# Kernel tuning notes

Measured on AMD Instinct MI355X. Metric: run time of the kernel, lower is better.

The kernel has to match this reference:

```python
import jax, jax.numpy as jnp
import numpy as np

ALPHA_MGD = 2e-05
NOISE_SIGMA = 8.0
NOISE_VAR = NOISE_SIGMA ** 2  # 64.0


def _conv2d(x, w, b, pad):
    # x: [N,C,H,W], w: [O,I,kh,kw]
    y = jax.lax.conv_general_dilated(
        x, w, window_strides=(1, 1), padding=[(pad, pad), (pad, pad)],
        dimension_numbers=("NCHW", "OIHW", "NCHW"))
    return y + b[None, :, None, None]


def setup_inputs() -> dict:
    key = jax.random.key(0)
    ks = jax.random.split(key, 8)
    N, Cs, Ct, H, W = 8, 128, 256, 64, 64
    return {
        "preds_S": jax.random.normal(ks[0], (N, Cs, H, W), jnp.float32),
        "preds_T": jax.random.normal(ks[1], (N, Ct, H, W), jnp.float32),
        "W_align": jax.random.normal(ks[2], (Ct, Cs, 1, 1), jnp.float32) * 0.05,
        "b_align": jnp.zeros((Ct,), jnp.float32),
        "W_gen1": jax.random.normal(ks[3], (Ct, Ct, 3, 3), jnp.float32) * 0.02,
        "b_gen1": jnp.zeros((Ct,), jnp.float32),
        "W_gen2": jax.random.normal(ks[4], (Ct, Ct, 3, 3), jnp.float32) * 0.02,
        "b_gen2": jnp.zeros((Ct,), jnp.float32),
    }


def reference(preds_S, preds_T, W_align, b_align, W_gen1, b_gen1, W_gen2, b_gen2):
    # align student channels to teacher channels (1x1 conv)
    s = _conv2d(preds_S, W_align, b_align, pad=0)
    N, C, H, W = preds_T.shape
    # deterministic checkerboard mask: tile([[0,1],[1,0]]) cropped to HxW -> (h+w) % 2
    hh = jnp.arange(H)[:, None]
    ww = jnp.arange(W)[None, :]
    mat = ((hh + ww) % 2).astype(s.dtype)  # [H,W]
    masked_fea = s * mat  # broadcast over [N,C,H,W]
    # generation network: conv3x3 -> relu -> conv3x3
    new_fea = _conv2d(jax.nn.relu(_conv2d(masked_fea, W_gen1, b_gen1, pad=1)), W_gen2, b_gen2, pad=1)
    # bmc_loss_md(pred=preds_T, target=new_fea, noise_var=64):
    # logits[i,j] = MVN(pred_i, noise_var*I).log_prob(target_j); the normalization
    # constant is class-independent and cancels in cross-entropy, keep the quadratic term.
    p = preds_T.reshape(N, -1)   # [N, D], D = C*H*W
    t = new_fea.reshape(N, -1)   # [N, D]
    # pairwise squared L2 via ||p||^2 + ||t||^2 - 2 p.t  (avoids NxNxD blow-up)
    sq = (jnp.sum(p * p, axis=1)[:, None]
          + jnp.sum(t * t, axis=1)[None, :]
          - 2.0 * (p @ t.T))  # [N, N]
    logits = -0.5 * sq / NOISE_VAR
    # cross_entropy(logits, arange(N)) = mean_i (logsumexp_j logits[i,j] - logits[i,i])
    ce = jnp.mean(jax.nn.logsumexp(logits, axis=1) - jnp.diagonal(logits))
    loss = ce * (2.0 * NOISE_VAR) / N
    return loss * ALPHA_MGD
```

## Files before the change

kernel.cpp:

```cpp
#include <hip/hip_runtime.h>

typedef unsigned short u16;
typedef short short8 __attribute__((ext_vector_type(8)));
typedef unsigned short ushort8 __attribute__((ext_vector_type(8)));
typedef float floatx16 __attribute__((ext_vector_type(16)));

#define PLANE8   34848
#define NSTRIDE  1115136

__device__ __forceinline__ u16 f2b(float f) {
  unsigned u = __builtin_bit_cast(unsigned, f);
  return (u16)((u + 0x7FFFu + ((u >> 16) & 1u)) >> 16);
}
__device__ __forceinline__ float b2f(u16 b) {
  return __builtin_bit_cast(float, ((unsigned)b) << 16);
}

typedef const __attribute__((address_space(1))) unsigned int* gptr_t;
typedef __attribute__((address_space(3))) unsigned int* sptr_t;

__global__ __launch_bounds__(256) void kprep(
    const float* __restrict__ Wg1, u16* __restrict__ Wsw1,
    const float* __restrict__ Wg2, u16* __restrict__ Wsw2,
    const float* __restrict__ Wa,  u16* __restrict__ Wb,
    const float* __restrict__ pS,  u16* __restrict__ T,
    u16* __restrict__ masked, u16* __restrict__ t1)
{
  __shared__ u16 Ls[64 * 136];
  int b = blockIdx.x, t = threadIdx.x;

  if (b < 576) {
    const float* W = (b < 288) ? Wg1 : Wg2;
    u16* D = (b < 288) ? Wsw1 : Wsw2;
    int bb = (b < 288) ? b : b - 288;
    int cid = bb * 256 + t;
    int d = cid % 1152, ctcg = cid / 1152;
    int ct = ctcg & 3, cg = ctcg >> 2;
    int colow = d & 31, cihalf = (d >> 5) & 1, sc = (d >> 6) & 1, tap = d >> 7;
    int co = ct * 64 + sc * 32 + colow;
    short8 v;
    #pragma unroll
    for (int jj = 0; jj < 8; ++jj) {
      int ci = cg * 16 + cihalf * 8 + jj;
      v[jj] = (short)f2b(W[((size_t)(co * 256 + ci)) * 9 + tap]);
    }
    *(short8*)&D[(size_t)cid * 8] = v;
  } else if (b < 592) {
    int v = (b - 576) * 256 + t;
    int colow = v & 31, hfb = (v >> 5) & 1, cog = (v >> 6) & 7, k = v >> 9;
    int co = cog * 32 + colow;
    int ci0 = k * 16 + hfb * 8;
    float4 f0 = *(const float4*)(Wa + (size_t)co * 128 + ci0);
    float4 f1 = *(const float4*)(Wa + (size_t)co * 128 + ci0 + 4);
    short8 o;
    o[0] = (short)f2b(f0.x); o[1] = (short)f2b(f0.y);
    o[2] = (short)f2b(f0.z); o[3] = (short)f2b(f0.w);
    o[4] = (short)f2b(f1.x); o[5] = (short)f2b(f1.y);
    o[6] = (short)f2b(f1.z); o[7] = (short)f2b(f1.w);
    *(short8*)&Wb[(size_t)v * 8] = o;
  } else if (b < 1104) {
    int bb = b - 592;
    int n = bb >> 6, pt = bb & 63, pix0 = pt * 64;
    int ci = t >> 1, ph = t & 1;
    const float* src = pS + ((size_t)n * 128 + ci) * 4096 + pix0 + ph * 32;
    #pragma unroll
    for (int i = 0; i < 8; ++i) {
      float4 v4 = *(const float4*)(src + i * 4);
      int pix = ph * 32 + i * 4;
      Ls[(pix + 0) * 136 + ci] = f2b(v4.x);
      Ls[(pix + 1) * 136 + ci] = f2b(v4.y);
      Ls[(pix + 2) * 136 + ci] = f2b(v4.z);
      Ls[(pix + 3) * 136 + ci] = f2b(v4.w);
    }
    __syncthreads();
    int p = t >> 2, q = t & 3;
    const u16* row = Ls + p * 136 + q * 32;
    u16* dst = T + ((size_t)n * 4096 + pix0 + p) * 128 + q * 32;
    #pragma unroll
    for (int k2 = 0; k2 < 4; ++k2)
      *(ushort8*)(dst + k2 * 8) = *(const ushort8*)(row + k2 * 8);
  } else {
    int p = b - 1104;
    u16* base = ((p >> 8) ? t1 : masked);
    int q = p & 255;
    base += (size_t)(q >> 5) * NSTRIDE + (size_t)(q & 31) * PLANE8;
    short8 z;
    #pragma unroll
    for (int jj = 0; jj < 8; ++jj) z[jj] = 0;
    #pragma unroll
    for (int pass = 0; pass < 2; ++pass) {
      int seg = t + pass * 256;
      if (seg < 264) {
        int off;
        if (seg < 66)       off = seg * 8;
        else if (seg < 132) off = (65 * 66 + (seg - 66)) * 8;
        else if (seg < 198) off = ((seg - 132) * 66) * 8;
        else                off = ((seg - 198) * 66 + 65) * 8;
        *(short8*)(base + off) = z;
      }
    }
  }
}

__global__ __launch_bounds__(256) void k1m(const u16* __restrict__ T,
    const u16* __restrict__ Wb, const float* __restrict__ ba,
    u16* __restrict__ mk)
{
  __shared__ __align__(16) u16 Wl[32768];
  int b = blockIdx.x;
  int n = b >> 5, pt = b & 31;
  int t = threadIdx.x, wid = t >> 6, lane = t & 63;
  int ml = lane & 31, hf = lane >> 5;

  #pragma unroll
  for (int kk = 0; kk < 16; ++kk) {
    int chunk = kk * 256 + t;
    __builtin_amdgcn_global_load_lds((gptr_t)(const void*)(Wb + (size_t)chunk * 8),
                                     (sptr_t)(void*)(Wl + chunk * 8), 16, 0, 0);
  }

  const u16* Tn = T + (size_t)n * 524288;
  const u16* ap[4];
  #pragma unroll
  for (int g = 0; g < 4; ++g)
    ap[g] = Tn + (size_t)(pt * 128 + g * 32 + ml) * 128 + hf * 8;

  floatx16 acc[2][4];
  #pragma unroll
  for (int q = 0; q < 2; ++q)
    #pragma unroll
    for (int g = 0; g < 4; ++g)
      #pragma unroll
      for (int i = 0; i < 16; ++i) acc[q][g][i] = 0.f;

  __syncthreads();

  const short8* WlV = (const short8*)Wl;
  int cogb = wid * 2;

  short8 a0[4], a1[4];
  #pragma unroll
  for (int g = 0; g < 4; ++g) a0[g] = *(const short8*)(ap[g]);

#define K1M_STEP(K, CUR, NXT, LAST)                                           \
  {                                                                           \
    if (!(LAST)) {                                                            \
      _Pragma("unroll")                                                       \
      for (int g = 0; g < 4; ++g)                                             \
        NXT[g] = *(const short8*)(ap[g] + ((K) + 1) * 16);                    \
    }                                                                         \
    short8 w0 = WlV[((K) * 8 + cogb) * 64 + lane];                            \
    short8 w1 = WlV[((K) * 8 + cogb + 1) * 64 + lane];                        \
    _Pragma("unroll")                                                         \
    for (int g = 0; g < 4; ++g) {                                             \
      acc[0][g] = __builtin_amdgcn_mfma_f32_32x32x16_bf16(CUR[g], w0, acc[0][g], 0, 0, 0); \
      acc[1][g] = __builtin_amdgcn_mfma_f32_32x32x16_bf16(CUR[g], w1, acc[1][g], 0, 0, 0); \
    }                                                                         \
  }
  K1M_STEP(0, a0, a1, 0)
  K1M_STEP(1, a1, a0, 0)
  K1M_STEP(2, a0, a1, 0)
  K1M_STEP(3, a1, a0, 0)
  K1M_STEP(4, a0, a1, 0)
  K1M_STEP(5, a1, a0, 0)
  K1M_STEP(6, a0, a1, 0)
  K1M_STEP(7, a1, a0, 1)
#undef K1M_STEP

  int co0 = cogb * 32 + ml, co1 = co0 + 32;
  float b0 = ba[co0], b1 = ba[co1];
  u16* base0 = mk + (size_t)n * NSTRIDE + (size_t)(co0 >> 3) * PLANE8 + (co0 & 7);
  u16* base1 = mk + (size_t)n * NSTRIDE + (size_t)(co1 >> 3) * PLANE8 + (co1 & 7);
  #pragma unroll
  for (int g = 0; g < 4; ++g)
    #pragma unroll
    for (int reg = 0; reg < 16; ++reg) {
      int m = (reg & 3) + 8 * (reg >> 2) + 4 * hf;
      int pix = pt * 128 + g * 32 + m;
      int h = pix >> 6, w = pix & 63;
      float msk = (float)((h + w) & 1);
      int off = ((h + 1) * 66 + (w + 1)) * 8;
      base0[off] = f2b((acc[0][g][reg] + b0) * msk);
      base1[off] = f2b((acc[1][g][reg] + b1) * msk);
    }
}

template <int MODE>
__global__ __launch_bounds__(256) void kconv(
    const u16* __restrict__ IN, const u16* __restrict__ WS,
    const float* __restrict__ bg, u16* __restrict__ OUT)
{
  __shared__ __align__(16) u16 LinA[896 * 8];
  __shared__ __align__(16) u16 LinB[896 * 8];
  __shared__ __align__(16) u16 LwA[1152 * 8];
  __shared__ __align__(16) u16 LwB[1152 * 8];

  int b = blockIdx.x;
  int rt = b & 15, ct = (b >> 4) & 3, n = b >> 6;
  int h0 = rt * 4;
  int t = threadIdx.x;
  int wid = t >> 6, lane = t & 63;
  int hf = lane >> 5, ml = lane & 31;

  const u16* inb = IN + (size_t)n * NSTRIDE;
  const u16* wg  = WS + (size_t)ct * 1152 * 8;

  floatx16 acc[2][2];
  #pragma unroll
  for (int s = 0; s < 2; ++s)
    #pragma unroll
    for (int q = 0; q < 2; ++q)
      #pragma unroll
      for (int i = 0; i < 16; ++i) acc[s][q][i] = 0.f;

  auto STAGE = [&](int cg, u16* LinD, u16* LwD) {
    #pragma unroll
    for (int k = 0; k < 5; ++k) {
      int sidx = 4 * k + wid;
      if (sidx < 18) {
        const u16* src = wg + (size_t)cg * 36864 + (size_t)(sidx * 64 + lane) * 8;
        __builtin_amdgcn_global_load_lds((gptr_t)(const void*)src,
                                         (sptr_t)(void*)(LwD + sidx * 512), 16, 0, 0);
      }
    }
    #pragma unroll
    for (int k = 0; k < 4; ++k) {
      int seg = 4 * k + wid;
      if (seg < 14) {
        int half = seg >= 7 ? 1 : 0;
        int s = seg - half * 7;
        const u16* src = inb + (size_t)cg * 69696 + half * PLANE8
                         + (size_t)(h0 * 66 + s * 64 + lane) * 8;
        __builtin_amdgcn_global_load_lds((gptr_t)(const void*)src,
                                         (sptr_t)(void*)(LinD + (half * 448 + s * 64) * 8),
                                         16, 0, 0);
      }
    }
  };

  auto COMPUTE = [&](const u16* LinS, const u16* LwS) {
    const short8* LinV = (const short8*)LinS;
    const short8* LwV  = (const short8*)LwS;
    #pragma unroll
    for (int dr = 0; dr < 3; ++dr) {
      int r0 = hf * 448 + (wid + dr) * 66;
      #pragma unroll
      for (int dc = 0; dc < 3; ++dc) {
        int tap = dr * 3 + dc;
        short8 w0 = LwV[tap * 128 + lane];
        short8 w1 = LwV[tap * 128 + 64 + lane];
        short8 i0 = LinV[r0 + ml + dc];
        short8 i1 = LinV[r0 + 32 + ml + dc];
        acc[0][0] = __builtin_amdgcn_mfma_f32_32x32x16_bf16(i0, w0, acc[0][0], 0, 0, 0);
        acc[0][1] = __builtin_amdgcn_mfma_f32_32x32x16_bf16(i0, w1, acc[0][1], 0, 0, 0);
        acc[1][0] = __builtin_amdgcn_mfma_f32_32x32x16_bf16(i1, w0, acc[1][0], 0, 0, 0);
        acc[1][1] = __builtin_amdgcn_mfma_f32_32x32x16_bf16(i1, w1, acc[1][1], 0, 0, 0);
      }
    }
  };

  STAGE(0, LinA, LwA);
  __syncthreads();
  for (int cg = 0; cg < 16; cg += 2) {
    STAGE(cg + 1, LinB, LwB);
    COMPUTE(LinA, LwA);
    __syncthreads();
    if (cg + 2 < 16) STAGE(cg + 2, LinA, LwA);
    COMPUTE(LinB, LwB);
    __syncthreads();
  }

  float bias0 = bg[ct * 64 + ml];
  float bias1 = bg[ct * 64 + 32 + ml];

  if (MODE == 0) {
    u16* ob = OUT + (size_t)n * NSTRIDE;
    int co0 = ct * 64 + ml, co1 = co0 + 32;
    int cb0 = ((co0 >> 4) * 2 + ((co0 >> 3) & 1)) * PLANE8 + (co0 & 7);
    int cb1 = ((co1 >> 4) * 2 + ((co1 >> 3) & 1)) * PLANE8 + (co1 & 7);
    int rowoff = (h0 + wid + 1) * 66 + 1;
    #pragma unroll
    for (int reg = 0; reg < 16; ++reg) {
      int m = (reg & 3) + 8 * (reg >> 2) + 4 * hf;
      float v;
      v = acc[0][0][reg] + bias0; v = fmaxf(v, 0.f); ob[cb0 + (rowoff + m) * 8] = f2b(v);
      v = acc[0][1][reg] + bias1; v = fmaxf(v, 0.f); ob[cb1 + (rowoff + m) * 8] = f2b(v);
      v = acc[1][0][reg] + bias0; v = fmaxf(v, 0.f); ob[cb0 + (rowoff + 32 + m) * 8] = f2b(v);
      v = acc[1][1][reg] + bias1; v = fmaxf(v, 0.f); ob[cb1 + (rowoff + 32 + m) * 8] = f2b(v);
    }
  } else {
    u16* plane;
    if (wid == 0)      plane = LinA;
    else if (wid == 1) plane = LinB;
    else if (wid == 2) plane = LwA;
    else               plane = LwA + 4352;
    #pragma unroll
    for (int reg = 0; reg < 16; ++reg) {
      int m = (reg & 3) + 8 * (reg >> 2) + 4 * hf;
      plane[ml * 68 + m]              = f2b(acc[0][0][reg] + bias0);
      plane[(32 + ml) * 68 + m]       = f2b(acc[0][1][reg] + bias1);
      plane[ml * 68 + 32 + m]         = f2b(acc[1][0][reg] + bias0);
      plane[(32 + ml) * 68 + 32 + m]  = f2b(acc[1][1][reg] + bias1);
    }
    const u16* row = plane + lane * 68;
    __align__(16) u16 tmp[64];
    #pragma unroll
    for (int k2 = 0; k2 < 16; ++k2)
      *(ushort4*)(tmp + k2 * 4) = *(const ushort4*)(row + k2 * 4);
    u16* gdst = OUT + (size_t)n * 1048576 + (size_t)(ct * 64 + lane) * 4096
                + (h0 + wid) * 64;
    #pragma unroll
    for (int k2 = 0; k2 < 8; ++k2)
      *(ushort8*)(gdst + k2 * 8) = *(const ushort8*)(tmp + k2 * 8);
  }
}

__global__ __launch_bounds__(256) void kbmc(const u16* __restrict__ t2,
    const float* __restrict__ pT, float* __restrict__ part)
{
  int t = threadIdx.x, lane = t & 63, role = t >> 6;
  int ih = role >> 1, nh = role & 1;
  int bid = blockIdx.x;

  float pt[4][4], pp[4], tt[4];
  #pragma unroll
  for (int i = 0; i < 4; ++i) {
    pp[i] = 0.f; tt[i] = 0.f;
    #pragma unroll
    for (int j = 0; j < 4; ++j) pt[i][j] = 0.f;
  }

  const float* pb = pT + ((size_t)ih * 4) * 1048576;
  const u16*   tb = t2 + ((size_t)nh * 4) * 1048576;

  for (int k = 0; k < 8; ++k) {
    size_t d0 = ((size_t)(bid * 512 + k * 64 + lane)) * 4;
    float4 p[4], tf[4];
    #pragma unroll
    for (int i = 0; i < 4; ++i)
      p[i] = *(const float4*)(pb + (size_t)i * 1048576 + d0);
    #pragma unroll
    for (int j = 0; j < 4; ++j) {
      ushort4 tv = *(const ushort4*)(tb + (size_t)j * 1048576 + d0);
      tf[j] = make_float4(b2f(tv.x), b2f(tv.y), b2f(tv.z), b2f(tv.w));
    }
    if (nh == 0) {
      #pragma unroll
      for (int i = 0; i < 4; ++i)
        pp[i] += p[i].x * p[i].x + p[i].y * p[i].y + p[i].z * p[i].z + p[i].w * p[i].w;
    }
    if (ih == 0) {
      #pragma unroll
      for (int j = 0; j < 4; ++j)
        tt[j] += tf[j].x * tf[j].x + tf[j].y * tf[j].y + tf[j].z * tf[j].z + tf[j].w * tf[j].w;
    }
    #pragma unroll
    for (int i = 0; i < 4; ++i)
      #pragma unroll
      for (int j = 0; j < 4; ++j)
        pt[i][j] += p[i].x * tf[j].x + p[i].y * tf[j].y
                  + p[i].z * tf[j].z + p[i].w * tf[j].w;
  }

  #pragma unroll
  for (int m = 1; m < 64; m <<= 1) {
    #pragma unroll
    for (int i = 0; i < 4; ++i) {
      pp[i] += __shfl_xor(pp[i], m);
      tt[i] += __shfl_xor(tt[i], m);
      #pragma unroll
      for (int j = 0; j < 4; ++j) pt[i][j] += __shfl_xor(pt[i][j], m);
    }
  }
  if (lane == 0) {
    #pragma unroll
    for (int i = 0; i < 4; ++i)
      #pragma unroll
      for (int j = 0; j < 4; ++j)
        part[(size_t)(16 + (ih * 4 + i) * 8 + (nh * 4 + j)) * 512 + bid] = pt[i][j];
    if (nh == 0) {
      #pragma unroll
      for (int i = 0; i < 4; ++i) part[(size_t)(ih * 4 + i) * 512 + bid] = pp[i];
    }
    if (ih == 0) {
      #pragma unroll
      for (int j = 0; j < 4; ++j) part[(size_t)(8 + nh * 4 + j) * 512 + bid] = tt[j];
    }
  }
}

__global__ __launch_bounds__(256) void k4f(const float* __restrict__ part,
                                           float* __restrict__ out)
{
  __shared__ float acs[96];
  int t = threadIdx.x, lane = t & 63, w = t >> 6;
  for (int s = w; s < 96; s += 4) {
    float v = 0.f;
    #pragma unroll
    for (int k = 0; k < 8; ++k) v += part[(size_t)s * 512 + k * 64 + lane];
    #pragma unroll
    for (int m = 1; m < 64; m <<= 1) v += __shfl_xor(v, m);
    if (lane == 0) acs[s] = v;
  }
  __syncthreads();
  if (t < 64) {
    int i = t >> 3, j = t & 7;
    double pp = acs[i];
    double tt = acs[8 + j];
    double pt = acs[16 + i * 8 + j];
    double logit = -0.5 * (pp + tt - 2.0 * pt) / 64.0;
    double m = logit;
    #pragma unroll
    for (int s = 1; s < 8; s <<= 1) {
      double o = __shfl_xor(m, s);
      m = o > m ? o : m;
    }
    double e = exp(logit - m);
    #pragma unroll
    for (int s = 1; s < 8; s <<= 1) e += __shfl_xor(e, s);
    double lse = m + log(e);
    double term = (j == i) ? (lse - logit) : 0.0;
    #pragma unroll
    for (int s = 1; s < 64; s <<= 1) term += __shfl_xor(term, s);
    if (t == 0) {
      double ce = term / 8.0;
      out[0] = (float)(ce * (2.0 * 64.0) / 8.0 * 2e-05);
    }
  }
}

extern "C" void kernel_launch(void* const* d_in, const int* in_sizes, int n_in,
                              void* d_out, int out_size, void* d_ws, size_t ws_size,
                              hipStream_t stream)
{
  const float* preds_S = (const float*)d_in[0];
  const float* preds_T = (const float*)d_in[1];
  const float* W_align = (const float*)d_in[2];
  const float* b_align = (const float*)d_in[3];
  const float* W_gen1  = (const float*)d_in[4];
  const float* b_gen1  = (const float*)d_in[5];
  const float* W_gen2  = (const float*)d_in[6];
  const float* b_gen2  = (const float*)d_in[7];
  float* out = (float*)d_out;

  char* wsb = (char*)d_ws;
  u16* masked = (u16*)wsb;
  u16* t1     = (u16*)(wsb + 17842176);
  u16* t2p    = (u16*)(wsb + 35684352);
  u16* T      = t2p;
  u16* Wsw1   = (u16*)(wsb + 52461568);
  u16* Wsw2   = (u16*)(wsb + 53641216);
  float* part   = (float*)(wsb + 54820864);
  float* accums = (float*)(wsb + 55017472);
  (void)accums;
  u16* Wb     = (u16*)(wsb + 55017856);

  kprep<<<1616, 256, 0, stream>>>(W_gen1, Wsw1, W_gen2, Wsw2, W_align, Wb,
                                  preds_S, T, masked, t1);
  k1m<<<256, 256, 0, stream>>>(T, Wb, b_align, masked);
  kconv<0><<<512, 256, 0, stream>>>(masked, Wsw1, b_gen1, t1);
  kconv<1><<<512, 256, 0, stream>>>(t1, Wsw2, b_gen2, t2p);
  kbmc<<<512, 256, 0, stream>>>(t2p, preds_T, part);
  k4f<<<1, 256, 0, stream>>>(part, out);
}
```

Before: 223.6 us.

## Enlarge conv row tile to 8 rows with 512-thread blocks; split final reduction

The 3x3 conv kernels now give each block 8 output rows and 8 waves instead of 4 rows and 4 waves, sharing one 40960-element LDS buffer. This halves the grid and cuts redundant weight staging and halo-row input loads per output row. The final loss kernel is split into a parallel 80-block partial-sum reduction plus a tiny 64-thread finalizer instead of one block looping over all slots. The cost is lower block-level parallelism (one 512-thread block per CU), more LDS per block, and an extra kernel launch.

```diff
diff --git a/kernel.cpp b/kernel.cpp
--- a/kernel.cpp
+++ b/kernel.cpp
@@ -186,18 +186,19 @@
 }
 
 template <int MODE>
-__global__ __launch_bounds__(256) void kconv(
+__global__ __launch_bounds__(512) void kconv(
     const u16* __restrict__ IN, const u16* __restrict__ WS,
     const float* __restrict__ bg, u16* __restrict__ OUT)
 {
-  __shared__ __align__(16) u16 LinA[896 * 8];
-  __shared__ __align__(16) u16 LinB[896 * 8];
-  __shared__ __align__(16) u16 LwA[1152 * 8];
-  __shared__ __align__(16) u16 LwB[1152 * 8];
+  __shared__ __align__(16) u16 L[40960];
+  u16* LinA = L;
+  u16* LwA  = L + 11264;
+  u16* LinB = L + 20480;
+  u16* LwB  = L + 31744;
 
   int b = blockIdx.x;
-  int rt = b & 15, ct = (b >> 4) & 3, n = b >> 6;
-  int h0 = rt * 4;
+  int rt = b & 7, ct = (b >> 3) & 3, n = b >> 5;
+  int h0 = rt * 8;
   int t = threadIdx.x;
   int wid = t >> 6, lane = t & 63;
   int hf = lane >> 5, ml = lane & 31;
@@ -215,8 +216,8 @@
 
   auto STAGE = [&](int cg, u16* LinD, u16* LwD) {
     #pragma unroll
-    for (int k = 0; k < 5; ++k) {
-      int sidx = 4 * k + wid;
+    for (int k = 0; k < 3; ++k) {
+      int sidx = 8 * k + wid;
       if (sidx < 18) {
         const u16* src = wg + (size_t)cg * 36864 + (size_t)(sidx * 64 + lane) * 8;
         __builtin_amdgcn_global_load_lds((gptr_t)(const void*)src,
@@ -224,15 +225,15 @@
       }
     }
     #pragma unroll
-    for (int k = 0; k < 4; ++k) {
-      int seg = 4 * k + wid;
-      if (seg < 14) {
-        int half = seg >= 7 ? 1 : 0;
-        int s = seg - half * 7;
+    for (int k = 0; k < 3; ++k) {
+      int seg = 8 * k + wid;
+      if (seg < 22) {
+        int half = seg >= 11 ? 1 : 0;
+        int s = seg - half * 11;
         const u16* src = inb + (size_t)cg * 69696 + half * PLANE8
                          + (size_t)(h0 * 66 + s * 64 + lane) * 8;
         __builtin_amdgcn_global_load_lds((gptr_t)(const void*)src,
-                                         (sptr_t)(void*)(LinD + (half * 448 + s * 64) * 8),
+                                         (sptr_t)(void*)(LinD + (half * 704 + s * 64) * 8),
                                          16, 0, 0);
       }
     }
@@ -243,7 +244,7 @@
     const short8* LwV  = (const short8*)LwS;
     #pragma unroll
     for (int dr = 0; dr < 3; ++dr) {
-      int r0 = hf * 448 + (wid + dr) * 66;
+      int r0 = hf * 704 + (wid + dr) * 66;
       #pragma unroll
       for (int dc = 0; dc < 3; ++dc) {
         int tap = dr * 3 + dc;
@@ -289,11 +290,7 @@
       v = acc[1][1][reg] + bias1; v = fmaxf(v, 0.f); ob[cb1 + (rowoff + 32 + m) * 8] = f2b(v);
     }
   } else {
-    u16* plane;
-    if (wid == 0)      plane = LinA;
-    else if (wid == 1) plane = LinB;
-    else if (wid == 2) plane = LwA;
-    else               plane = LwA + 4352;
+    u16* plane = L + wid * 4352;
     #pragma unroll
     for (int reg = 0; reg < 16; ++reg) {
       int m = (reg & 3) + 8 * (reg >> 2) + 4 * hf;
@@ -389,43 +386,43 @@
   }
 }
 
-__global__ __launch_bounds__(256) void k4f(const float* __restrict__ part,
-                                           float* __restrict__ out)
-{
-  __shared__ float acs[96];
-  int t = threadIdx.x, lane = t & 63, w = t >> 6;
-  for (int s = w; s < 96; s += 4) {
-    float v = 0.f;
-    #pragma unroll
-    for (int k = 0; k < 8; ++k) v += part[(size_t)s * 512 + k * 64 + lane];
-    #pragma unroll
-    for (int m = 1; m < 64; m <<= 1) v += __shfl_xor(v, m);
-    if (lane == 0) acs[s] = v;
-  }
+__global__ __launch_bounds__(256) void kred(const float* __restrict__ part,
+                                            float* __restrict__ accums)
+{
+  __shared__ float r4[4];
+  int s = blockIdx.x, t = threadIdx.x, lane = t & 63, wid = t >> 6;
+  float v = part[(size_t)s * 512 + t] + part[(size_t)s * 512 + 256 + t];
+  #pragma unroll
+  for (int m = 1; m < 64; m <<= 1) v += __shfl_xor(v, m);
+  if (lane == 0) r4[wid] = v;
   __syncthreads();
-  if (t < 64) {
-    int i = t >> 3, j = t & 7;
-    double pp = acs[i];
-    double tt = acs[8 + j];
-    double pt = acs[16 + i * 8 + j];
-    double logit = -0.5 * (pp + tt - 2.0 * pt) / 64.0;
-    double m = logit;
-    #pragma unroll
-    for (int s = 1; s < 8; s <<= 1) {
-      double o = __shfl_xor(m, s);
-      m = o > m ? o : m;
-    }
-    double e = exp(logit - m);
-    #pragma unroll
-    for (int s = 1; s < 8; s <<= 1) e += __shfl_xor(e, s);
-    double lse = m + log(e);
-    double term = (j == i) ? (lse - logit) : 0.0;
-    #pragma unroll
-    for (int s = 1; s < 64; s <<= 1) term += __shfl_xor(term, s);
-    if (t == 0) {
-      double ce = term / 8.0;
-      out[0] = (float)(ce * (2.0 * 64.0) / 8.0 * 2e-05);
-    }
+  if (t == 0) accums[s] = r4[0] + r4[1] + r4[2] + r4[3];
+}
+
+__global__ void k4_final(const float* __restrict__ accums, float* __restrict__ out)
+{
+  int t = threadIdx.x;
+  int i = t >> 3, j = t & 7;
+  double pp = accums[i];
+  double tt = accums[8 + j];
+  double pt = accums[16 + i * 8 + j];
+  double logit = -0.5 * (pp + tt - 2.0 * pt) / 64.0;
+  double m = logit;
+  #pragma unroll
+  for (int s = 1; s < 8; s <<= 1) {
+    double o = __shfl_xor(m, s);
+    m = o > m ? o : m;
+  }
+  double e = exp(logit - m);
+  #pragma unroll
+  for (int s = 1; s < 8; s <<= 1) e += __shfl_xor(e, s);
+  double lse = m + log(e);
+  double term = (j == i) ? (lse - logit) : 0.0;
+  #pragma unroll
+  for (int s = 1; s < 64; s <<= 1) term += __shfl_xor(term, s);
+  if (t == 0) {
+    double ce = term / 8.0;
+    out[0] = (float)(ce * (2.0 * 64.0) / 8.0 * 2e-05);
   }
 }
 
@@ -452,14 +449,14 @@
   u16* Wsw2   = (u16*)(wsb + 53641216);
   float* part   = (float*)(wsb + 54820864);
   float* accums = (float*)(wsb + 55017472);
-  (void)accums;
   u16* Wb     = (u16*)(wsb + 55017856);
 
   kprep<<<1616, 256, 0, stream>>>(W_gen1, Wsw1, W_gen2, Wsw2, W_align, Wb,
                                   preds_S, T, masked, t1);
   k1m<<<256, 256, 0, stream>>>(T, Wb, b_align, masked);
-  kconv<0><<<512, 256, 0, stream>>>(masked, Wsw1, b_gen1, t1);
-  kconv<1><<<512, 256, 0, stream>>>(t1, Wsw2, b_gen2, t2p);
+  kconv<0><<<256, 512, 0, stream>>>(masked, Wsw1, b_gen1, t1);
+  kconv<1><<<256, 512, 0, stream>>>(t1, Wsw2, b_gen2, t2p);
   kbmc<<<512, 256, 0, stream>>>(t2p, preds_T, part);
-  k4f<<<1, 256, 0, stream>>>(part, out);
-}
+  kred<<<80, 256, 0, stream>>>(part, accums);
+  k4_final<<<1, 64, 0, stream>>>(accums, out);
+}
```

After: 208.0 us, median of 2. 1.07x faster.
